# Kernel optimization log

Hardware: AMD Instinct MI355X
Metric: run time of the kernel (lower is better)

## Reference

```python
import jax, jax.numpy as jnp
import numpy as np

NUM_NEURONS = 256
NUM_SAMPLES = 512
MAX_SPIKES = 32
N_STEPS = 32          # fixed RK4 steps per spike round (stands in for adaptive Tsit5)
ALPHA = 0.03
V_RESET = 1.0
T0 = 0.0


def setup_inputs() -> dict:
    key = jax.random.key(0)
    ks = jax.random.split(key, 7)
    input_current = jax.random.normal(ks[0], (NUM_NEURONS,), dtype=jnp.float32)
    # _build_w with network=all-False: uniform(minval=0.5), mask sets nothing
    w = jax.random.uniform(ks[1], (NUM_NEURONS, NUM_NEURONS), minval=0.5, maxval=1.0, dtype=jnp.float32)
    mu = jax.random.uniform(ks[2], (2,), minval=0.5, maxval=1.0, dtype=jnp.float32)
    v0 = jax.random.normal(ks[3], (NUM_NEURONS,), dtype=jnp.float32)
    i0 = jax.random.normal(ks[4], (NUM_NEURONS,), dtype=jnp.float32)
    # s0 = log(U) - alpha  (always < 0)
    s0 = (jnp.log(jax.random.uniform(ks[5], (NUM_SAMPLES, NUM_NEURONS), minval=1e-6, maxval=1.0)) - ALPHA).astype(jnp.float32)
    # pre-drawn stochastic resets, one per (spike round, sample, neuron)
    reset_s = (jnp.log(jax.random.uniform(ks[6], (MAX_SPIKES, NUM_SAMPLES, NUM_NEURONS), minval=1e-6, maxval=1.0)) - ALPHA).astype(jnp.float32)
    return dict(input_current=input_current, w=w, mu=mu, v0=v0, i0=i0, s0=s0, reset_s=reset_s, t1=2)


def _drift(y, ic, mu1, mu2):
    # y: [samples, neurons, 3] = (v, i, s)
    v, i = y[..., 0], y[..., 1]
    dv = mu1 * (i + ic - v)
    di = -mu2 * i
    ds = jax.nn.sigmoid(v)  # intensity_fn(v)
    return jnp.stack([dv, di, ds], axis=-1)


def reference(input_current, w, mu, v0, i0, s0, reset_s, t1):
    t1f = jnp.float32(t1)
    mu1, mu2 = mu[0], mu[1]
    ic = input_current  # constant-in-time input current, [neurons]

    y0 = jnp.concatenate([
        jnp.broadcast_to(v0, (NUM_SAMPLES, NUM_NEURONS))[..., None],
        jnp.broadcast_to(i0, (NUM_SAMPLES, NUM_NEURONS))[..., None],
        s0[..., None]], axis=-1)  # [samples, neurons, 3]

    def rk4(y, h):
        k1 = _drift(y, ic, mu1, mu2)
        k2 = _drift(y + 0.5 * h * k1, ic, mu1, mu2)
        k3 = _drift(y + 0.5 * h * k2, ic, mu1, mu2)
        k4 = _drift(y + h * k3, ic, mu1, mu2)
        return y + (h / 6.0) * (k1 + 2.0 * k2 + 2.0 * k3 + k4)

    def round_body(carry, reset_k):
        t0s, y_in = carry                      # t0s: [samples]
        dt = (t1f - t0s) / N_STEPS             # per-sample step size
        h = dt[:, None, None]

        def step(sc, _):
            t, y, done, tev, yev, emask = sc
            y_new = rk4(y, h)
            y_new = jnp.where(done[:, None, None], y, y_new)  # freeze after event
            s_prev, s_new = y[..., 2], y_new[..., 2]
            crossed = s_new > 0.0                              # cond_fn root: s crosses 0
            trig = crossed.any(axis=1) & (~done)
            idx = jnp.argmax(s_new, axis=1)                    # event neuron (first/largest crossing)
            sp = jnp.take_along_axis(s_prev, idx[:, None], 1)[:, 0]
            sn = jnp.take_along_axis(s_new, idx[:, None], 1)[:, 0]
            frac = jnp.clip(sp / (sp - sn + 1e-12), 0.0, 1.0)  # linear root estimate (Newton stand-in)
            t_c = t + frac * dt
            y_c = y + frac[:, None, None] * (y_new - y)
            tev = jnp.where(trig, t_c, tev)
            yev = jnp.where(trig[:, None, None], y_c, yev)
            emask = jnp.where(trig[:, None], crossed, emask)
            y = jnp.where(trig[:, None, None], y_c, y_new)
            done = done | trig
            return (t + dt, y, done, tev, yev, emask), None

        done0 = jnp.zeros((NUM_SAMPLES,), bool)
        tev0 = jnp.full((NUM_SAMPLES,), jnp.inf, jnp.float32)
        em0 = jnp.zeros((NUM_SAMPLES, NUM_NEURONS), bool)
        (_, yend, done, tev, yev, emask), _ = jax.lax.scan(
            step, (t0s, y_in, done0, tev0, y_in, em0), None, length=N_STEPS)

        tev = jnp.where(done, tev, t1f)                 # no event -> sol.ts[-1] = t1
        yev = jnp.where(done[:, None, None], yev, yend)

        # trans_fn: spike reset + synaptic jump w[event_idx]
        eidx = jnp.argmax(emask, axis=1)
        w_row = jnp.where(done[:, None], w[eidx], 0.0)  # zero if no event happened
        v_t = yev[..., 0] - jnp.where(emask, V_RESET, 0.0)
        i_t = yev[..., 1] + w_row
        s_t = jnp.minimum(jnp.where(emask, reset_k, yev[..., 2]), 0.0)
        y_next = jnp.stack([v_t, i_t, s_t], axis=-1)
        return (tev, y_next), (tev, yev, emask)

    t0s = jnp.full((NUM_SAMPLES,), T0, jnp.float32)
    _, (tevs, yevs, emasks) = jax.lax.scan(jax.checkpoint(round_body), (t0s, y0), reset_s)

    spike_times = jnp.transpose(tevs, (1, 0))            # [samples, max_spikes]
    spike_values = jnp.transpose(yevs, (1, 0, 2, 3))     # [samples, max_spikes, neurons, 3]
    spike_marks = jnp.transpose(emasks, (1, 0, 2))       # [samples, max_spikes, neurons]
    return spike_times, spike_values, spike_marks
```

## Files before the change

### kernel.cpp

```cpp
#include <hip/hip_runtime.h>
#include <math.h>

#define NN 256
#define NS 512
#define MS 32
#define NSTEP 32
#define VRESET 1.0f

__device__ __forceinline__ float sigf(float x) {
    float e = __expf(-x);
    return __builtin_amdgcn_rcpf(1.0f + e);
}

__global__ __launch_bounds__(256) void snn_kernel(
    const float* __restrict__ ic_g,
    const float* __restrict__ w,
    const float* __restrict__ mu,
    const float* __restrict__ v0,
    const float* __restrict__ i0,
    const float* __restrict__ s0,
    const float* __restrict__ reset_s,
    const int*   __restrict__ t1p,
    float* __restrict__ out)
{
    const int tid  = threadIdx.x;
    const int lane = tid & 63;
    const int wid  = tid >> 6;
    const int samp = blockIdx.x;
    const float mu1 = mu[0];
    const float mu2 = mu[1];
    const float t1f = (float)t1p[0];

    __shared__ int   s_any[2][4];
    __shared__ float s_bv[4], s_bsp[4];
    __shared__ int   s_bn[4];
    __shared__ int   s_eidx[4];

    float v  = v0[tid];
    float ii = i0[tid];
    float s  = s0[samp * NN + tid];
    const float ic = ic_g[tid];
    float t0 = 0.0f;

    float* times = out;
    float* vals  = out + (size_t)NS * MS;
    float* marks = out + (size_t)NS * MS * (1 + NN * 3);

    for (int r = 0; r < MS; ++r) {
        const float dt = (t1f - t0) / (float)NSTEP;
        float tev = t1f;
        float yev_v, yev_i, yev_s;
        bool  em = false;
        bool  done = false;

        if (dt != 0.0f) {
            float t = t0;
            const float hh = 0.5f * dt;
            const float h6 = dt * (1.0f / 6.0f);
            for (int st = 0; st < NSTEP; ++st) {
                float kv1 = mu1 * (ii + ic - v);
                float ki1 = -mu2 * ii;
                float ks1 = sigf(v);
                float v2 = v + hh * kv1;
                float i2 = ii + hh * ki1;
                float kv2 = mu1 * (i2 + ic - v2);
                float ki2 = -mu2 * i2;
                float ks2 = sigf(v2);
                float v3 = v + hh * kv2;
                float i3 = ii + hh * ki2;
                float kv3 = mu1 * (i3 + ic - v3);
                float ki3 = -mu2 * i3;
                float ks3 = sigf(v3);
                float v4 = v + dt * kv3;
                float i4 = ii + dt * ki3;
                float kv4 = mu1 * (i4 + ic - v4);
                float ki4 = -mu2 * i4;
                float ks4 = sigf(v4);
                float vn = v  + h6 * (kv1 + 2.0f * kv2 + 2.0f * kv3 + kv4);
                float in_ = ii + h6 * (ki1 + 2.0f * ki2 + 2.0f * ki3 + ki4);
                float sn = s  + h6 * (ks1 + 2.0f * ks2 + 2.0f * ks3 + ks4);

                unsigned long long bl = __ballot(sn > 0.0f);
                if (lane == 0) s_any[st & 1][wid] = (bl != 0ull) ? 1 : 0;
                __syncthreads();
                int anyflag = s_any[st & 1][0] | s_any[st & 1][1] |
                              s_any[st & 1][2] | s_any[st & 1][3];

                if (anyflag) {
                    float bv = sn, bsp = s;
                    int   bn = tid;
#pragma unroll
                    for (int off = 32; off >= 1; off >>= 1) {
                        float ov  = __shfl_xor(bv, off);
                        float osp = __shfl_xor(bsp, off);
                        int   on  = __shfl_xor(bn, off);
                        if (ov > bv || (ov == bv && on < bn)) { bv = ov; bsp = osp; bn = on; }
                    }
                    if (lane == 0) { s_bv[wid] = bv; s_bsp[wid] = bsp; s_bn[wid] = bn; }
                    __syncthreads();
                    bv = s_bv[0]; bsp = s_bsp[0]; bn = s_bn[0];
#pragma unroll
                    for (int wv = 1; wv < 4; ++wv) {
                        float ov = s_bv[wv], osp = s_bsp[wv];
                        int   on = s_bn[wv];
                        if (ov > bv || (ov == bv && on < bn)) { bv = ov; bsp = osp; bn = on; }
                    }
                    float frac = bsp / (bsp - bv + 1e-12f);
                    frac = fminf(fmaxf(frac, 0.0f), 1.0f);
                    tev = t + frac * dt;
                    yev_v = v  + frac * (vn - v);
                    yev_i = ii + frac * (in_ - ii);
                    yev_s = s  + frac * (sn - s);
                    em = sn > 0.0f;
                    v = yev_v; ii = yev_i; s = yev_s;
                    done = true;
                    break;
                }
                v = vn; ii = in_; s = sn;
                t += dt;
            }
        }

        if (!done) {
            tev = t1f;
            yev_v = v; yev_i = ii; yev_s = s; em = false;
        }

        const int sr = samp * MS + r;
        if (tid == 0) times[sr] = tev;
        {
            float* p = vals + ((size_t)sr * NN + tid) * 3;
            p[0] = yev_v;
            p[1] = yev_i;
            p[2] = yev_s;
            marks[(size_t)sr * NN + tid] = em ? 1.0f : 0.0f;
        }

        if (done) {
            unsigned long long bm = __ballot(em);
            int cand = (bm != 0ull) ? (wid * 64 + (int)__builtin_ctzll(bm)) : (2 * NN);
            if (lane == 0) s_eidx[wid] = cand;
            __syncthreads();
            int eidx = s_eidx[0];
            eidx = (s_eidx[1] < eidx) ? s_eidx[1] : eidx;
            eidx = (s_eidx[2] < eidx) ? s_eidx[2] : eidx;
            eidx = (s_eidx[3] < eidx) ? s_eidx[3] : eidx;

            float wr = w[eidx * NN + tid];
            v  = yev_v - (em ? VRESET : 0.0f);
            ii = yev_i + wr;
            float sres = em ? reset_s[((size_t)r * NS + samp) * NN + tid] : yev_s;
            s = fminf(sres, 0.0f);
        } else {
            s = fminf(s, 0.0f);
        }
        t0 = tev;
    }
}

extern "C" void kernel_launch(void* const* d_in, const int* in_sizes, int n_in,
                              void* d_out, int out_size, void* d_ws, size_t ws_size,
                              hipStream_t stream) {
    const float* ic      = (const float*)d_in[0];
    const float* w       = (const float*)d_in[1];
    const float* mu      = (const float*)d_in[2];
    const float* v0      = (const float*)d_in[3];
    const float* i0      = (const float*)d_in[4];
    const float* s0      = (const float*)d_in[5];
    const float* reset_s = (const float*)d_in[6];
    const int*   t1p     = (const int*)d_in[7];
    float* out = (float*)d_out;

    snn_kernel<<<dim3(NS), dim3(256), 0, stream>>>(ic, w, mu, v0, i0, s0,
                                                   reset_s, t1p, out);
}
```

Before: 154.3 us.

## Software-pipeline RK4 steps past the barrier and fuse event-index reduction

Computes the next RK4 step speculatively before the block barrier, so the ALU work overlaps the cross-wave any-crossing check, and replaces __syncthreads with a lighter LDS-only wait plus s_barrier. The argmax reduction now packs the value and index into one 64-bit key, so each shuffle step moves one value instead of three, and the event-index ballot is folded into the same barrier phase. The w-row and reset_s loads are issued earlier to hide their latency. In exchange, the last speculative step is wasted work whenever a crossing occurs, and the code uses more registers.

```diff
diff --git a/kernel.cpp b/kernel.cpp
--- a/kernel.cpp
+++ b/kernel.cpp
@@ -10,6 +10,40 @@
 __device__ __forceinline__ float sigf(float x) {
     float e = __expf(-x);
     return __builtin_amdgcn_rcpf(1.0f + e);
+}
+
+__device__ __forceinline__ void block_sync_lds() {
+    asm volatile("s_waitcnt lgkmcnt(0)" ::: "memory");
+    __builtin_amdgcn_s_barrier();
+    asm volatile("" ::: "memory");
+}
+
+__device__ __forceinline__ void rk4step(float v, float ii, float s,
+                                        float ic, float mu1, float mu2,
+                                        float dt, float hh, float h6,
+                                        float& vn, float& in_, float& sn)
+{
+    float kv1 = mu1 * (ii + ic - v);
+    float ki1 = -mu2 * ii;
+    float ks1 = sigf(v);
+    float v2 = v + hh * kv1;
+    float i2 = ii + hh * ki1;
+    float kv2 = mu1 * (i2 + ic - v2);
+    float ki2 = -mu2 * i2;
+    float ks2 = sigf(v2);
+    float v3 = v + hh * kv2;
+    float i3 = ii + hh * ki2;
+    float kv3 = mu1 * (i3 + ic - v3);
+    float ki3 = -mu2 * i3;
+    float ks3 = sigf(v3);
+    float v4 = v + dt * kv3;
+    float i4 = ii + dt * ki3;
+    float kv4 = mu1 * (i4 + ic - v4);
+    float ki4 = -mu2 * i4;
+    float ks4 = sigf(v4);
+    vn  = v  + h6 * (kv1 + 2.0f * kv2 + 2.0f * kv3 + kv4);
+    in_ = ii + h6 * (ki1 + 2.0f * ki2 + 2.0f * ki3 + ki4);
+    sn  = s  + h6 * (ks1 + 2.0f * ks2 + 2.0f * ks3 + ks4);
 }
 
 __global__ __launch_bounds__(256) void snn_kernel(
@@ -31,9 +65,10 @@
     const float mu2 = mu[1];
     const float t1f = (float)t1p[0];
 
-    __shared__ int   s_any[2][4];
-    __shared__ float s_bv[4], s_bsp[4];
-    __shared__ int   s_bn[4];
+    __shared__ int   s_any[4][4];
+    __shared__ float s_sn[NN];
+    __shared__ float s_sp[NN];
+    __shared__ unsigned long long s_key[4];
     __shared__ int   s_eidx[4];
 
     float v  = v0[tid];
@@ -47,112 +82,114 @@
     float* marks = out + (size_t)NS * MS * (1 + NN * 3);
 
     for (int r = 0; r < MS; ++r) {
+        const float rs = reset_s[((size_t)r * NS + samp) * NN + tid];
+
         const float dt = (t1f - t0) / (float)NSTEP;
         float tev = t1f;
-        float yev_v, yev_i, yev_s;
+        float yv = v, yi = ii, ys = s;
         bool  em = false;
         bool  done = false;
+        float wr = 0.0f;
 
         if (dt != 0.0f) {
-            float t = t0;
             const float hh = 0.5f * dt;
             const float h6 = dt * (1.0f / 6.0f);
+
+            float pv = v, pi_ = ii, ps = s;
+            float cv, ci, cs;
+            rk4step(pv, pi_, ps, ic, mu1, mu2, dt, hh, h6, cv, ci, cs);
+            float t = t0;
+
             for (int st = 0; st < NSTEP; ++st) {
-                float kv1 = mu1 * (ii + ic - v);
-                float ki1 = -mu2 * ii;
-                float ks1 = sigf(v);
-                float v2 = v + hh * kv1;
-                float i2 = ii + hh * ki1;
-                float kv2 = mu1 * (i2 + ic - v2);
-                float ki2 = -mu2 * i2;
-                float ks2 = sigf(v2);
-                float v3 = v + hh * kv2;
-                float i3 = ii + hh * ki2;
-                float kv3 = mu1 * (i3 + ic - v3);
-                float ki3 = -mu2 * i3;
-                float ks3 = sigf(v3);
-                float v4 = v + dt * kv3;
-                float i4 = ii + dt * ki3;
-                float kv4 = mu1 * (i4 + ic - v4);
-                float ki4 = -mu2 * i4;
-                float ks4 = sigf(v4);
-                float vn = v  + h6 * (kv1 + 2.0f * kv2 + 2.0f * kv3 + kv4);
-                float in_ = ii + h6 * (ki1 + 2.0f * ki2 + 2.0f * ki3 + ki4);
-                float sn = s  + h6 * (ks1 + 2.0f * ks2 + 2.0f * ks3 + ks4);
-
-                unsigned long long bl = __ballot(sn > 0.0f);
-                if (lane == 0) s_any[st & 1][wid] = (bl != 0ull) ? 1 : 0;
-                __syncthreads();
-                int anyflag = s_any[st & 1][0] | s_any[st & 1][1] |
-                              s_any[st & 1][2] | s_any[st & 1][3];
-
-                if (anyflag) {
-                    float bv = sn, bsp = s;
-                    int   bn = tid;
+                unsigned long long bl = __ballot(cs > 0.0f);
+                if (lane == 0) s_any[st & 3][wid] = (bl != 0ull) ? 1 : 0;
+
+                float nv = 0.0f, ni = 0.0f, ns_ = 0.0f;
+                const bool notlast = (st + 1 < NSTEP);
+                if (notlast)
+                    rk4step(cv, ci, cs, ic, mu1, mu2, dt, hh, h6, nv, ni, ns_);
+
+                block_sync_lds();
+                int af = s_any[st & 3][0] | s_any[st & 3][1] |
+                         s_any[st & 3][2] | s_any[st & 3][3];
+
+                if (af) {
+                    bool crossed = cs > 0.0f;
+                    s_sn[tid] = cs;
+                    s_sp[tid] = ps;
+
+                    unsigned int b = __float_as_uint(cs);
+                    unsigned int m = (b & 0x80000000u) ? 0xFFFFFFFFu : 0x80000000u;
+                    unsigned long long key =
+                        ((unsigned long long)(b ^ m) << 32) |
+                        (unsigned int)(NN - 1 - tid);
 #pragma unroll
                     for (int off = 32; off >= 1; off >>= 1) {
-                        float ov  = __shfl_xor(bv, off);
-                        float osp = __shfl_xor(bsp, off);
-                        int   on  = __shfl_xor(bn, off);
-                        if (ov > bv || (ov == bv && on < bn)) { bv = ov; bsp = osp; bn = on; }
+                        unsigned long long o = __shfl_xor(key, off);
+                        key = (o > key) ? o : key;
                     }
-                    if (lane == 0) { s_bv[wid] = bv; s_bsp[wid] = bsp; s_bn[wid] = bn; }
-                    __syncthreads();
-                    bv = s_bv[0]; bsp = s_bsp[0]; bn = s_bn[0];
-#pragma unroll
-                    for (int wv = 1; wv < 4; ++wv) {
-                        float ov = s_bv[wv], osp = s_bsp[wv];
-                        int   on = s_bn[wv];
-                        if (ov > bv || (ov == bv && on < bn)) { bv = ov; bsp = osp; bn = on; }
-                    }
+                    unsigned long long bm = __ballot(crossed);
+                    int cand = (bm != 0ull)
+                                   ? (wid * 64 + (int)__builtin_ctzll(bm))
+                                   : (2 * NN);
+                    if (lane == 0) { s_key[wid] = key; s_eidx[wid] = cand; }
+                    block_sync_lds();
+
+                    unsigned long long k0 = s_key[0], k1 = s_key[1];
+                    unsigned long long k2 = s_key[2], k3 = s_key[3];
+                    k0 = (k1 > k0) ? k1 : k0;
+                    k2 = (k3 > k2) ? k3 : k2;
+                    k0 = (k2 > k0) ? k2 : k0;
+                    int bn = NN - 1 - (int)(unsigned int)(k0 & 0xFFFFFFFFull);
+
+                    int eidx = s_eidx[0];
+                    eidx = (s_eidx[1] < eidx) ? s_eidx[1] : eidx;
+                    eidx = (s_eidx[2] < eidx) ? s_eidx[2] : eidx;
+                    eidx = (s_eidx[3] < eidx) ? s_eidx[3] : eidx;
+
+                    wr = w[eidx * NN + tid];
+
+                    float bv  = s_sn[bn];
+                    float bsp = s_sp[bn];
                     float frac = bsp / (bsp - bv + 1e-12f);
                     frac = fminf(fmaxf(frac, 0.0f), 1.0f);
                     tev = t + frac * dt;
-                    yev_v = v  + frac * (vn - v);
-                    yev_i = ii + frac * (in_ - ii);
-                    yev_s = s  + frac * (sn - s);
-                    em = sn > 0.0f;
-                    v = yev_v; ii = yev_i; s = yev_s;
+                    yv = pv  + frac * (cv - pv);
+                    yi = pi_ + frac * (ci - pi_);
+                    ys = ps  + frac * (cs - ps);
+                    em = crossed;
                     done = true;
                     break;
                 }
-                v = vn; ii = in_; s = sn;
-                t += dt;
+
+                if (notlast) {
+                    pv = cv; pi_ = ci; ps = cs;
+                    cv = nv; ci = ni; cs = ns_;
+                    t += dt;
+                }
             }
-        }
-
-        if (!done) {
-            tev = t1f;
-            yev_v = v; yev_i = ii; yev_s = s; em = false;
+
+            if (!done) { yv = cv; yi = ci; ys = cs; }
         }
 
         const int sr = samp * MS + r;
         if (tid == 0) times[sr] = tev;
         {
             float* p = vals + ((size_t)sr * NN + tid) * 3;
-            p[0] = yev_v;
-            p[1] = yev_i;
-            p[2] = yev_s;
+            p[0] = yv;
+            p[1] = yi;
+            p[2] = ys;
             marks[(size_t)sr * NN + tid] = em ? 1.0f : 0.0f;
         }
 
         if (done) {
-            unsigned long long bm = __ballot(em);
-            int cand = (bm != 0ull) ? (wid * 64 + (int)__builtin_ctzll(bm)) : (2 * NN);
-            if (lane == 0) s_eidx[wid] = cand;
-            __syncthreads();
-            int eidx = s_eidx[0];
-            eidx = (s_eidx[1] < eidx) ? s_eidx[1] : eidx;
-            eidx = (s_eidx[2] < eidx) ? s_eidx[2] : eidx;
-            eidx = (s_eidx[3] < eidx) ? s_eidx[3] : eidx;
-
-            float wr = w[eidx * NN + tid];
-            v  = yev_v - (em ? VRESET : 0.0f);
-            ii = yev_i + wr;
-            float sres = em ? reset_s[((size_t)r * NS + samp) * NN + tid] : yev_s;
+            v  = yv - (em ? VRESET : 0.0f);
+            ii = yi + wr;
+            float sres = em ? rs : ys;
             s = fminf(sres, 0.0f);
         } else {
-            s = fminf(s, 0.0f);
+            v = yv; ii = yi;
+            s = fminf(ys, 0.0f);
         }
         t0 = tev;
     }
```

Result: faster. 143.6 us (-6.9%).

## Use one wavefront per sample to eliminate block barriers in RK4 loop

Applied to the files above, without the earlier changes.

Each sample now runs in a single 64-lane wavefront that holds four neurons per lane in registers, instead of a 256-thread block with one neuron per thread. The per-step any-crossing check and the argmax now use wave ballots and shuffles rather than shared memory and __syncthreads. The argmax is done on order-preserving integer keys. The reset_s row and the w row are fetched ahead of use to hide their latency. In exchange, each lane does four times the serial RK4 work, and the grid has only 512 waves, so the GPU has less parallelism to hide latency.

```diff
diff --git a/kernel.cpp b/kernel.cpp
--- a/kernel.cpp
+++ b/kernel.cpp
@@ -12,7 +12,35 @@
     return __builtin_amdgcn_rcpf(1.0f + e);
 }
 
-__global__ __launch_bounds__(256) void snn_kernel(
+__device__ __forceinline__ void rk4step(float v, float ii, float s,
+                                        float ic, float mu1, float mu2,
+                                        float dt, float hh, float h6,
+                                        float& vn, float& in_, float& sn)
+{
+    float kv1 = mu1 * (ii + ic - v);
+    float ki1 = -mu2 * ii;
+    float ks1 = sigf(v);
+    float v2 = v + hh * kv1;
+    float i2 = ii + hh * ki1;
+    float kv2 = mu1 * (i2 + ic - v2);
+    float ki2 = -mu2 * i2;
+    float ks2 = sigf(v2);
+    float v3 = v + hh * kv2;
+    float i3 = ii + hh * ki2;
+    float kv3 = mu1 * (i3 + ic - v3);
+    float ki3 = -mu2 * i3;
+    float ks3 = sigf(v3);
+    float v4 = v + dt * kv3;
+    float i4 = ii + dt * ki3;
+    float kv4 = mu1 * (i4 + ic - v4);
+    float ki4 = -mu2 * i4;
+    float ks4 = sigf(v4);
+    vn  = v  + h6 * (kv1 + 2.0f * kv2 + 2.0f * kv3 + kv4);
+    in_ = ii + h6 * (ki1 + 2.0f * ki2 + 2.0f * ki3 + ki4);
+    sn  = s  + h6 * (ks1 + 2.0f * ks2 + 2.0f * ks3 + ks4);
+}
+
+__global__ __launch_bounds__(64) void snn_kernel(
     const float* __restrict__ ic_g,
     const float* __restrict__ w,
     const float* __restrict__ mu,
@@ -23,23 +51,21 @@
     const int*   __restrict__ t1p,
     float* __restrict__ out)
 {
-    const int tid  = threadIdx.x;
-    const int lane = tid & 63;
-    const int wid  = tid >> 6;
+    const int lane = threadIdx.x;
     const int samp = blockIdx.x;
     const float mu1 = mu[0];
     const float mu2 = mu[1];
     const float t1f = (float)t1p[0];
 
-    __shared__ int   s_any[2][4];
-    __shared__ float s_bv[4], s_bsp[4];
-    __shared__ int   s_bn[4];
-    __shared__ int   s_eidx[4];
-
-    float v  = v0[tid];
-    float ii = i0[tid];
-    float s  = s0[samp * NN + tid];
-    const float ic = ic_g[tid];
+    float vv[4], ii[4], ss[4], ic[4];
+#pragma unroll
+    for (int q = 0; q < 4; ++q) {
+        const int n = q * 64 + lane;
+        vv[q] = v0[n];
+        ii[q] = i0[n];
+        ss[q] = s0[samp * NN + n];
+        ic[q] = ic_g[n];
+    }
     float t0 = 0.0f;
 
     float* times = out;
@@ -47,112 +73,139 @@
     float* marks = out + (size_t)NS * MS * (1 + NN * 3);
 
     for (int r = 0; r < MS; ++r) {
+        float rs[4];
+#pragma unroll
+        for (int q = 0; q < 4; ++q)
+            rs[q] = reset_s[((size_t)r * NS + samp) * NN + q * 64 + lane];
+
         const float dt = (t1f - t0) / (float)NSTEP;
         float tev = t1f;
-        float yev_v, yev_i, yev_s;
-        bool  em = false;
+        float yv[4], yi[4], ys[4];
+        bool  em[4] = {false, false, false, false};
+        float wr[4] = {0.0f, 0.0f, 0.0f, 0.0f};
         bool  done = false;
 
         if (dt != 0.0f) {
-            float t = t0;
             const float hh = 0.5f * dt;
             const float h6 = dt * (1.0f / 6.0f);
+            float t = t0;
+
             for (int st = 0; st < NSTEP; ++st) {
-                float kv1 = mu1 * (ii + ic - v);
-                float ki1 = -mu2 * ii;
-                float ks1 = sigf(v);
-                float v2 = v + hh * kv1;
-                float i2 = ii + hh * ki1;
-                float kv2 = mu1 * (i2 + ic - v2);
-                float ki2 = -mu2 * i2;
-                float ks2 = sigf(v2);
-                float v3 = v + hh * kv2;
-                float i3 = ii + hh * ki2;
-                float kv3 = mu1 * (i3 + ic - v3);
-                float ki3 = -mu2 * i3;
-                float ks3 = sigf(v3);
-                float v4 = v + dt * kv3;
-                float i4 = ii + dt * ki3;
-                float kv4 = mu1 * (i4 + ic - v4);
-                float ki4 = -mu2 * i4;
-                float ks4 = sigf(v4);
-                float vn = v  + h6 * (kv1 + 2.0f * kv2 + 2.0f * kv3 + kv4);
-                float in_ = ii + h6 * (ki1 + 2.0f * ki2 + 2.0f * ki3 + ki4);
-                float sn = s  + h6 * (ks1 + 2.0f * ks2 + 2.0f * ks3 + ks4);
-
-                unsigned long long bl = __ballot(sn > 0.0f);
-                if (lane == 0) s_any[st & 1][wid] = (bl != 0ull) ? 1 : 0;
-                __syncthreads();
-                int anyflag = s_any[st & 1][0] | s_any[st & 1][1] |
-                              s_any[st & 1][2] | s_any[st & 1][3];
-
-                if (anyflag) {
-                    float bv = sn, bsp = s;
-                    int   bn = tid;
+                float vn[4], inn[4], sn[4];
+#pragma unroll
+                for (int q = 0; q < 4; ++q)
+                    rk4step(vv[q], ii[q], ss[q], ic[q], mu1, mu2,
+                            dt, hh, h6, vn[q], inn[q], sn[q]);
+
+                const bool anyc = (sn[0] > 0.0f) | (sn[1] > 0.0f) |
+                                  (sn[2] > 0.0f) | (sn[3] > 0.0f);
+                if (__ballot(anyc) != 0ull) {
+                    unsigned long long b0 = __ballot(sn[0] > 0.0f);
+                    unsigned long long b1 = __ballot(sn[1] > 0.0f);
+                    unsigned long long b2 = __ballot(sn[2] > 0.0f);
+                    unsigned long long b3 = __ballot(sn[3] > 0.0f);
+                    int eidx;
+                    if (b0)      eidx =       (int)__builtin_ctzll(b0);
+                    else if (b1) eidx =  64 + (int)__builtin_ctzll(b1);
+                    else if (b2) eidx = 128 + (int)__builtin_ctzll(b2);
+                    else         eidx = 192 + (int)__builtin_ctzll(b3);
+
+#pragma unroll
+                    for (int q = 0; q < 4; ++q)
+                        wr[q] = w[eidx * NN + q * 64 + lane];
+
+                    unsigned k0, k1, k2, k3;
+                    {
+                        unsigned b;
+                        b = __float_as_uint(sn[0]);
+                        k0 = (b & 0x80000000u) ? ~b : (b | 0x80000000u);
+                        b = __float_as_uint(sn[1]);
+                        k1 = (b & 0x80000000u) ? ~b : (b | 0x80000000u);
+                        b = __float_as_uint(sn[2]);
+                        k2 = (b & 0x80000000u) ? ~b : (b | 0x80000000u);
+                        b = __float_as_uint(sn[3]);
+                        k3 = (b & 0x80000000u) ? ~b : (b | 0x80000000u);
+                    }
+                    unsigned ka = k0 > k1 ? k0 : k1;
+                    unsigned kb = k2 > k3 ? k2 : k3;
+                    unsigned red = ka > kb ? ka : kb;
 #pragma unroll
                     for (int off = 32; off >= 1; off >>= 1) {
-                        float ov  = __shfl_xor(bv, off);
-                        float osp = __shfl_xor(bsp, off);
-                        int   on  = __shfl_xor(bn, off);
-                        if (ov > bv || (ov == bv && on < bn)) { bv = ov; bsp = osp; bn = on; }
+                        unsigned o = __shfl_xor(red, off);
+                        red = (o > red) ? o : red;
                     }
-                    if (lane == 0) { s_bv[wid] = bv; s_bsp[wid] = bsp; s_bn[wid] = bn; }
-                    __syncthreads();
-                    bv = s_bv[0]; bsp = s_bsp[0]; bn = s_bn[0];
-#pragma unroll
-                    for (int wv = 1; wv < 4; ++wv) {
-                        float ov = s_bv[wv], osp = s_bsp[wv];
-                        int   on = s_bn[wv];
-                        if (ov > bv || (ov == bv && on < bn)) { bv = ov; bsp = osp; bn = on; }
-                    }
+                    unsigned long long c0 = __ballot(k0 == red);
+                    unsigned long long c1 = __ballot(k1 == red);
+                    unsigned long long c2 = __ballot(k2 == red);
+                    unsigned long long c3 = __ballot(k3 == red);
+                    int qw, lw;
+                    if (c0)      { qw = 0; lw = (int)__builtin_ctzll(c0); }
+                    else if (c1) { qw = 1; lw = (int)__builtin_ctzll(c1); }
+                    else if (c2) { qw = 2; lw = (int)__builtin_ctzll(c2); }
+                    else         { qw = 3; lw = (int)__builtin_ctzll(c3); }
+
+                    float bv, bsp;
+                    if (qw == 0)      { bv = __shfl(sn[0], lw); bsp = __shfl(ss[0], lw); }
+                    else if (qw == 1) { bv = __shfl(sn[1], lw); bsp = __shfl(ss[1], lw); }
+                    else if (qw == 2) { bv = __shfl(sn[2], lw); bsp = __shfl(ss[2], lw); }
+                    else              { bv = __shfl(sn[3], lw); bsp = __shfl(ss[3], lw); }
+
                     float frac = bsp / (bsp - bv + 1e-12f);
                     frac = fminf(fmaxf(frac, 0.0f), 1.0f);
                     tev = t + frac * dt;
-                    yev_v = v  + frac * (vn - v);
-                    yev_i = ii + frac * (in_ - ii);
-                    yev_s = s  + frac * (sn - s);
-                    em = sn > 0.0f;
-                    v = yev_v; ii = yev_i; s = yev_s;
+#pragma unroll
+                    for (int q = 0; q < 4; ++q) {
+                        yv[q] = vv[q] + frac * (vn[q]  - vv[q]);
+                        yi[q] = ii[q] + frac * (inn[q] - ii[q]);
+                        ys[q] = ss[q] + frac * (sn[q]  - ss[q]);
+                        em[q] = sn[q] > 0.0f;
+                    }
                     done = true;
                     break;
                 }
-                v = vn; ii = in_; s = sn;
+
+#pragma unroll
+                for (int q = 0; q < 4; ++q) {
+                    vv[q] = vn[q]; ii[q] = inn[q]; ss[q] = sn[q];
+                }
                 t += dt;
             }
         }
 
         if (!done) {
-            tev = t1f;
-            yev_v = v; yev_i = ii; yev_s = s; em = false;
+#pragma unroll
+            for (int q = 0; q < 4; ++q) {
+                yv[q] = vv[q]; yi[q] = ii[q]; ys[q] = ss[q];
+            }
         }
 
         const int sr = samp * MS + r;
-        if (tid == 0) times[sr] = tev;
-        {
-            float* p = vals + ((size_t)sr * NN + tid) * 3;
-            p[0] = yev_v;
-            p[1] = yev_i;
-            p[2] = yev_s;
-            marks[(size_t)sr * NN + tid] = em ? 1.0f : 0.0f;
+        if (lane == 0) times[sr] = tev;
+#pragma unroll
+        for (int q = 0; q < 4; ++q) {
+            const int n = q * 64 + lane;
+            float* p = vals + ((size_t)sr * NN + n) * 3;
+            p[0] = yv[q];
+            p[1] = yi[q];
+            p[2] = ys[q];
+            marks[(size_t)sr * NN + n] = em[q] ? 1.0f : 0.0f;
         }
 
         if (done) {
-            unsigned long long bm = __ballot(em);
-            int cand = (bm != 0ull) ? (wid * 64 + (int)__builtin_ctzll(bm)) : (2 * NN);
-            if (lane == 0) s_eidx[wid] = cand;
-            __syncthreads();
-            int eidx = s_eidx[0];
-            eidx = (s_eidx[1] < eidx) ? s_eidx[1] : eidx;
-            eidx = (s_eidx[2] < eidx) ? s_eidx[2] : eidx;
-            eidx = (s_eidx[3] < eidx) ? s_eidx[3] : eidx;
-
-            float wr = w[eidx * NN + tid];
-            v  = yev_v - (em ? VRESET : 0.0f);
-            ii = yev_i + wr;
-            float sres = em ? reset_s[((size_t)r * NS + samp) * NN + tid] : yev_s;
-            s = fminf(sres, 0.0f);
+#pragma unroll
+            for (int q = 0; q < 4; ++q) {
+                vv[q] = yv[q] - (em[q] ? VRESET : 0.0f);
+                ii[q] = yi[q] + wr[q];
+                float sres = em[q] ? rs[q] : ys[q];
+                ss[q] = fminf(sres, 0.0f);
+            }
         } else {
-            s = fminf(s, 0.0f);
+#pragma unroll
+            for (int q = 0; q < 4; ++q) {
+                vv[q] = yv[q];
+                ii[q] = yi[q];
+                ss[q] = fminf(ys[q], 0.0f);
+            }
         }
         t0 = tev;
     }
@@ -171,6 +224,6 @@
     const int*   t1p     = (const int*)d_in[7];
     float* out = (float*)d_out;
 
-    snn_kernel<<<dim3(NS), dim3(256), 0, stream>>>(ic, w, mu, v0, i0, s0,
-                                                   reset_s, t1p, out);
-}
+    snn_kernel<<<dim3(NS), dim3(64), 0, stream>>>(ic, w, mu, v0, i0, s0,
+                                                  reset_s, t1p, out);
+}
```

Measured after the change: 141.2 us. -8.5%, faster.
